# Kernel optimization log

Hardware: AMD Instinct MI355X
Metric: run time of the kernel (lower is better)

## Reference

```python
import jax, jax.numpy as jnp
import numpy as np
from jax import lax

N, S, H, L, E, V = 10000, 20, 512, 2, 100000, 10000


def setup_inputs() -> dict:
    key = jax.random.key(0)
    ks = jax.random.split(key, 12)
    return {
        "emb": jax.random.normal(ks[0], (V, H), jnp.float32),
        "W_ir": jax.random.normal(ks[1], (L, H, H), jnp.float32) * (2.0 / H) ** 0.5,
        "b_ir": jnp.ones((L, H), jnp.float32),
        "W_iz": jax.random.normal(ks[2], (L, H, H), jnp.float32) * (2.0 / H) ** 0.5,
        "b_iz": jnp.ones((L, H), jnp.float32),
        "lin_w": jax.random.normal(ks[3], (1, H), jnp.float32) * (1.0 / H) ** 0.5,
        "lin_b": jnp.zeros((1,), jnp.float32),
        "skip_w": jax.random.uniform(ks[4], (H, H), jnp.float32),
        "skip_b": jax.random.uniform(ks[5], (H,), jnp.float32),
        "walk_idx": jax.random.randint(ks[6], (N, S), 0, V),
        "edge_label_index": jax.random.randint(ks[7], (2, E), 0, N),
    }


def reference(emb, W_ir, b_ir, W_iz, b_iz, lin_w, lin_b, skip_w, skip_b,
              walk_idx, edge_label_index):
    x = emb[walk_idx]                       # [N, S, H]
    hn = jnp.zeros((x.shape[0], emb.shape[1]), x.dtype)
    for l in range(W_ir.shape[0]):
        # gates depend only on x, precompute all steps: F.linear(x, W) = x @ W.T
        h_all = jnp.einsum('nsh,kh->snk', x, W_ir[l]) + b_ir[l]          # [S, N, H]
        z_all = jax.nn.sigmoid(jnp.einsum('nsh,kh->snk', x, W_iz[l]) + b_iz[l])

        def step(h, tz):
            ht, zt = tz
            return (1.0 - zt) * h + zt * ht, None

        hn, _ = lax.scan(step, hn, (h_all, z_all))
    # note: F.dropout result in original is dead (overwritten); omitted
    score = jax.nn.sigmoid(hn @ lin_w.T + lin_b)        # [N, 1]
    node_feat = score[edge_label_index]                  # [2, E, 1]
    pred = jnp.sum(node_feat[0] * node_feat[1], axis=-1)  # [E] ('dot' decode)
    out2 = hn @ skip_w.T + skip_b                        # [N, H]
    return pred, out2
```

## Files before the change

### kernel.cpp

```cpp
#include <hip/hip_runtime.h>

#define H  512
#define NN 10000
#define SS 20
#define VV 100000
#define EE 100000

typedef __bf16 bf16x8 __attribute__((ext_vector_type(8)));
typedef float  f32x4  __attribute__((ext_vector_type(4)));

__device__ __forceinline__ unsigned short f2bf(float f) {
  unsigned u = __builtin_bit_cast(unsigned, f);
  u += 0x7FFFu + ((u >> 16) & 1u);
  return (unsigned short)(u >> 16);
}
__device__ __forceinline__ float bflo(int x) {
  return __builtin_bit_cast(float, (unsigned)x << 16);
}
__device__ __forceinline__ float bfhi(int x) {
  return __builtin_bit_cast(float, (unsigned)x & 0xFFFF0000u);
}
__device__ __forceinline__ float sigm(float x) { return 1.f / (1.f + __expf(-x)); }

__device__ __forceinline__ unsigned cpk(float lo, float hi) {
  unsigned r;
  asm("v_cvt_pk_bf16_f32 %0, %1, %2" : "=v"(r) : "v"(lo), "v"(hi));
  return r;
}
__device__ __forceinline__ void cvt_store8(unsigned short* dst, float4 a, float4 b) {
  int4 v;
  v.x = (int)cpk(a.x, a.y); v.y = (int)cpk(a.z, a.w);
  v.z = (int)cpk(b.x, b.y); v.w = (int)cpk(b.z, b.w);
  *(int4*)dst = v;
}
__device__ __forceinline__ bf16x8 cvt8(float4 a, float4 b) {
  int4 v;
  v.x = (int)cpk(a.x, a.y); v.y = (int)cpk(a.z, a.w);
  v.z = (int)cpk(b.x, b.y); v.w = (int)cpk(b.z, b.w);
  return __builtin_bit_cast(bf16x8, v);
}

__device__ __forceinline__ void pub_barrier() {
  asm volatile("s_waitcnt lgkmcnt(0)\n\ts_barrier" ::: "memory");
}

__launch_bounds__(256, 2)
__global__ void gru_fused(const float* __restrict__ emb,
                          const float* __restrict__ W_ir,
                          const float* __restrict__ W_iz,
                          const float* __restrict__ b_ir,
                          const float* __restrict__ b_iz,
                          const int* __restrict__ walk,
                          unsigned short* __restrict__ hnb) {
  __shared__ unsigned short As[4][80 * 64];
  __shared__ unsigned short hout[2][4][32];

  const int tid = threadIdx.x;
  const int w = tid >> 6, lane = tid & 63;
  const int r = lane & 15, q = lane >> 4;

  const int hwid = blockIdx.y * 16 + blockIdx.x;
  const int cg = (hwid >> 3) & 15;
  const int sb = ((hwid & 7) << 2) + (hwid >> 7);
  const int c0 = cg * 32;

  const int ly = r & 1;
  const int cch = c0 + 8 * w + (r >> 1);
  bf16x8 barr[2][16];
  float bias2[2];
  #pragma unroll
  for (int t = 0; t < 2; ++t) {
    const float* wrow = (t ? W_iz : W_ir) + (long)ly * H * H + (long)cch * H;
    #pragma unroll
    for (int u = 0; u < 16; ++u) {
      const float* s = wrow + u * 32 + q * 8;
      barr[t][u] = cvt8(*(const float4*)s, *(const float4*)(s + 4));
    }
    bias2[t] = (t ? b_iz : b_ir)[ly * H + cch];
  }

  const int row0 = tid >> 3, g0 = tid & 7;
  const int row1 = row0 + 32, row2 = row0 + 64;
  const bool has2 = (tid < 128);
  #define LMAP(m) (20 * (((m) >> 2) & 3) + 4 * ((m) >> 4) + ((m) & 3))
  #define SWZ(m)  ((m) * 64 + ((g0 ^ ((m) & 7)) * 8))
  const int L0 = LMAP(row0), L1 = LMAP(row1), L2 = LMAP(row2);
  const int sw0 = SWZ(row0), sw1 = SWZ(row1), sw2 = SWZ(row2);

  const int ngA = (2500 * sb) >> 5;
  const int ngB = (2500 * (sb + 1)) >> 5;

  int v0 = walk[ngA * 80 + L0]; v0 = ((unsigned)v0 < VV) ? v0 : 0;
  int v1 = walk[ngA * 80 + L1]; v1 = ((unsigned)v1 < VV) ? v1 : 0;
  int cur0 = v0 * H, cur1 = v1 * H, cur2 = 0;
  if (has2) { int v2 = walk[ngA * 80 + L2]; v2 = ((unsigned)v2 < VV) ? v2 : 0; cur2 = v2 * H; }

  float4 p0a[2], p0b[2], p1a[2], p1b[2], p2a[2], p2b[2];
  p2a[0] = p2a[1] = p2b[0] = p2b[1] = (float4){0, 0, 0, 0};

  {
    const float* s0 = emb + cur0 + g0 * 8;
    const float* s1 = emb + cur1 + g0 * 8;
    const float* s2 = emb + cur2 + g0 * 8;
    float4 a0 = *(const float4*)s0, b0 = *(const float4*)(s0 + 4);
    float4 a1 = *(const float4*)s1, b1 = *(const float4*)(s1 + 4);
    float4 a2 = {0,0,0,0}, b2 = {0,0,0,0};
    if (has2) { a2 = *(const float4*)s2; b2 = *(const float4*)(s2 + 4); }
    cvt_store8(&As[0][sw0], a0, b0);
    cvt_store8(&As[0][sw1], a1, b1);
    if (has2) cvt_store8(&As[0][sw2], a2, b2);
    a0 = *(const float4*)(s0 + 64); b0 = *(const float4*)(s0 + 68);
    a1 = *(const float4*)(s1 + 64); b1 = *(const float4*)(s1 + 68);
    if (has2) { a2 = *(const float4*)(s2 + 64); b2 = *(const float4*)(s2 + 68); }
    cvt_store8(&As[1][sw0], a0, b0);
    cvt_store8(&As[1][sw1], a1, b1);
    if (has2) cvt_store8(&As[1][sw2], a2, b2);
    p0a[0] = *(const float4*)(s0 + 128); p0b[0] = *(const float4*)(s0 + 132);
    p1a[0] = *(const float4*)(s1 + 128); p1b[0] = *(const float4*)(s1 + 132);
    if (has2) { p2a[0] = *(const float4*)(s2 + 128); p2b[0] = *(const float4*)(s2 + 132); }
  }

  f32x4 acc[5][2];
  const f32x4 fz = {0.f, 0.f, 0.f, 0.f};

  for (int ng = ngA; ng < ngB; ++ng) {
    #pragma unroll
    for (int mt = 0; mt < 5; ++mt)
      #pragma unroll
      for (int t = 0; t < 2; ++t) acc[mt][t] = fz;

    const int ngn = (ng + 1 < ngB) ? ng + 1 : ng;
    int n0 = walk[ngn * 80 + L0]; n0 = ((unsigned)n0 < VV) ? n0 : 0;
    int n1 = walk[ngn * 80 + L1]; n1 = ((unsigned)n1 < VV) ? n1 : 0;
    const int nxt0 = n0 * H, nxt1 = n1 * H;
    int nxt2 = 0;
    if (has2) { int n2 = walk[ngn * 80 + L2]; n2 = ((unsigned)n2 < VV) ? n2 : 0; nxt2 = n2 * H; }

    #pragma unroll
    for (int kc = 0; kc < 8; ++kc) {
      if ((kc & 1) == 0) pub_barrier();

      {
        const int cix = kc + 3;
        const int off = (cix & 7) * 64;
        const int u0 = (cix < 8) ? cur0 : nxt0;
        const int u1 = (cix < 8) ? cur1 : nxt1;
        const float* s0 = emb + u0 + off + g0 * 8;
        p0a[cix & 1] = *(const float4*)s0; p0b[cix & 1] = *(const float4*)(s0 + 4);
        const float* s1 = emb + u1 + off + g0 * 8;
        p1a[cix & 1] = *(const float4*)s1; p1b[cix & 1] = *(const float4*)(s1 + 4);
        if (has2) {
          const int u2 = (cix < 8) ? cur2 : nxt2;
          const float* s2 = emb + u2 + off + g0 * 8;
          p2a[cix & 1] = *(const float4*)s2; p2b[cix & 1] = *(const float4*)(s2 + 4);
        }
      }

      {
        unsigned short* An = &As[(kc + 2) & 3][0];
        cvt_store8(&An[sw0], p0a[kc & 1], p0b[kc & 1]);
        cvt_store8(&An[sw1], p1a[kc & 1], p1b[kc & 1]);
        if (has2) cvt_store8(&An[sw2], p2a[kc & 1], p2b[kc & 1]);
      }

      const unsigned short* Ab = &As[kc & 3][0];
      #pragma unroll
      for (int ks = 0; ks < 2; ++ks) {
        bf16x8 a[5];
        #pragma unroll
        for (int mt = 0; mt < 5; ++mt) {
          const int ar = mt * 16 + r;
          a[mt] = *(const bf16x8*)&Ab[ar * 64 + (((ks * 4 + q) ^ (ar & 7)) * 8)];
        }
        #pragma unroll
        for (int mt = 0; mt < 5; ++mt)
          #pragma unroll
          for (int t = 0; t < 2; ++t)
            acc[mt][t] = __builtin_amdgcn_mfma_f32_16x16x32_bf16(
                a[mt], barr[t][kc * 2 + ks], acc[mt][t], 0, 0, 0);
      }
    }

    {
      float hn1 = 0.f, a2 = 1.f, b2 = 0.f;
      #pragma unroll
      for (int s = 0; s < 20; ++s) {
        const float yh = acc[s >> 2][0][s & 3] + bias2[0];
        const float yz = acc[s >> 2][1][s & 3] + bias2[1];
        const float z = sigm(yz);
        hn1 += z * (yh - hn1);
        a2 *= (1.f - z);
        b2 += z * (yh - b2);
      }
      const float u2 = __shfl_xor(hn1, 1);
      if (ly == 1) hout[ng & 1][q][8 * w + (r >> 1)] = f2bf(a2 * u2 + b2);
    }
    pub_barrier();
    if (tid < 16) {
      const int nd = tid >> 2, seg = tid & 3;
      int4 v = *(const int4*)&hout[ng & 1][nd][seg * 8];
      *(int4*)(hnb + (long)(ng * 4 + nd) * 1024 + c0 + seg * 8) = v;
    }
    cur0 = nxt0; cur1 = nxt1; cur2 = nxt2;
  }
}

__global__ void score_kernel(const unsigned short* __restrict__ hnb,
                             const float* __restrict__ lin_w,
                             const float* __restrict__ lin_b,
                             float* __restrict__ R) {
  int tid = threadIdx.x;
  int wv = tid >> 6, lane = tid & 63;
  int node = blockIdx.x * 4 + wv;
  int k = lane * 8;
  int4 hv = *(const int4*)(hnb + (long)node * 1024 + k);
  float4 w0 = *(const float4*)(lin_w + k);
  float4 w1 = *(const float4*)(lin_w + k + 4);
  float s = bflo(hv.x) * w0.x + bfhi(hv.x) * w0.y + bflo(hv.y) * w0.z + bfhi(hv.y) * w0.w
          + bflo(hv.z) * w1.x + bfhi(hv.z) * w1.y + bflo(hv.w) * w1.z + bfhi(hv.w) * w1.w;
  #pragma unroll
  for (int off = 32; off > 0; off >>= 1) s += __shfl_down(s, off);
  if (lane == 0) R[256 + (long)node * 512] = sigm(s + lin_b[0]);
}

__global__ void pred_kernel(const int* __restrict__ eli, const float* __restrict__ R,
                            float* __restrict__ out) {
  int e = blockIdx.x * 256 + threadIdx.x;
  if (e < EE) {
    int a = eli[e];       a = (unsigned)a < NN ? a : 0;
    int b = eli[EE + e];  b = (unsigned)b < NN ? b : 0;
    out[e] = R[256 + (long)a * 512] * R[256 + (long)b * 512];
  }
}

__launch_bounds__(256)
__global__ void out2_kernel(const unsigned short* __restrict__ hnb,
                            const float* __restrict__ skip_w,
                            const float* __restrict__ skip_b,
                            float* __restrict__ out2) {
  __shared__ unsigned short Asl[32][520];
  __shared__ unsigned short Bsl[512][40];
  const int tid = threadIdx.x;
  const int lane = tid & 63, wv = tid >> 6;
  const int r = lane & 15, q = lane >> 4;
  const int m0 = blockIdx.x * 32;

  {
    int arow = tid >> 4;
    int acol = (tid & 15) * 32;
    #pragma unroll
    for (int hh = 0; hh < 2; ++hh) {
      int grow = m0 + hh * 16 + arow;
      unsigned short* dst = &Asl[hh * 16 + arow][acol];
      if (grow < NN) {
        const unsigned short* hr = hnb + (long)grow * 1024 + acol;
        *(int4*)(dst)      = *(const int4*)(hr);
        *(int4*)(dst + 8)  = *(const int4*)(hr + 8);
        *(int4*)(dst + 16) = *(const int4*)(hr + 16);
        *(int4*)(dst + 24) = *(const int4*)(hr + 24);
      } else {
        int4 z = {0, 0, 0, 0};
        *(int4*)(dst) = z; *(int4*)(dst + 8) = z;
        *(int4*)(dst + 16) = z; *(int4*)(dst + 24) = z;
      }
    }
  }

  const f32x4 fzero = {0.f, 0.f, 0.f, 0.f};
  f32x4 acc[2][8];
  #pragma unroll
  for (int rg = 0; rg < 2; ++rg)
    #pragma unroll
    for (int i = 0; i < 8; ++i) acc[rg][i] = fzero;

  const int ksub = (tid & 3) * 8;
  const int jb = tid >> 2;

  for (int k0 = 0; k0 < H; k0 += 32) {
    __syncthreads();
    #pragma unroll
    for (int it = 0; it < 8; ++it) {
      int jj = it * 64 + jb;
      const float* src = skip_w + (long)jj * H + k0 + ksub;
      cvt_store8(&Bsl[jj][ksub], *(const float4*)src, *(const float4*)(src + 4));
    }
    __syncthreads();
    bf16x8 af0 = *(const bf16x8*)&Asl[r][k0 + q * 8];
    bf16x8 af1 = *(const bf16x8*)&Asl[16 + r][k0 + q * 8];
    #pragma unroll
    for (int i = 0; i < 8; ++i) {
      bf16x8 bf = *(const bf16x8*)&Bsl[(wv * 8 + i) * 16 + r][q * 8];
      acc[0][i] = __builtin_amdgcn_mfma_f32_16x16x32_bf16(af0, bf, acc[0][i], 0, 0, 0);
      acc[1][i] = __builtin_amdgcn_mfma_f32_16x16x32_bf16(af1, bf, acc[1][i], 0, 0, 0);
    }
  }
  #pragma unroll
  for (int rg = 0; rg < 2; ++rg)
    #pragma unroll
    for (int i = 0; i < 8; ++i) {
      int col = (wv * 8 + i) * 16 + r;
      float sbv = skip_b[col];
      #pragma unroll
      for (int g = 0; g < 4; ++g) {
        int grow = m0 + rg * 16 + q * 4 + g;
        if (grow < NN) out2[(long)grow * H + col] = acc[rg][i][g] + sbv;
      }
    }
}

extern "C" void kernel_launch(void* const* d_in, const int* in_sizes, int n_in,
                              void* d_out, int out_size, void* d_ws, size_t ws_size,
                              hipStream_t stream) {
  const float* emb    = (const float*)d_in[0];
  const float* W_ir   = (const float*)d_in[1];
  const float* b_ir   = (const float*)d_in[2];
  const float* W_iz   = (const float*)d_in[3];
  const float* b_iz   = (const float*)d_in[4];
  const float* lin_w  = (const float*)d_in[5];
  const float* lin_b  = (const float*)d_in[6];
  const float* skip_w = (const float*)d_in[7];
  const float* skip_b = (const float*)d_in[8];
  const int*   walk   = (const int*)d_in[9];
  const int*   eli    = (const int*)d_in[10];
  float* out = (float*)d_out;
  float* R   = out + EE;
  unsigned short* hnb = (unsigned short*)R;

  dim3 g1(16, 32);
  gru_fused<<<g1, 256, 0, stream>>>(emb, W_ir, W_iz, b_ir, b_iz, walk, hnb);
  score_kernel<<<2500, 256, 0, stream>>>(hnb, lin_w, lin_b, R);
  pred_kernel<<<391, 256, 0, stream>>>(eli, R, out);
  out2_kernel<<<313, 256, 0, stream>>>(hnb, skip_w, skip_b, R);
}
```

Measured before the change: 680.2 us.

## Switch GRU gate GEMM to FP8 MFMA with more blocks per CU

Result: slower. 703.6 us (+3.4%).

```diff
diff --git a/kernel.cpp b/kernel.cpp
--- a/kernel.cpp
+++ b/kernel.cpp
@@ -33,18 +33,20 @@
   v.z = (int)cpk(b.x, b.y); v.w = (int)cpk(b.z, b.w);
   *(int4*)dst = v;
 }
-__device__ __forceinline__ bf16x8 cvt8(float4 a, float4 b) {
-  int4 v;
-  v.x = (int)cpk(a.x, a.y); v.y = (int)cpk(a.z, a.w);
-  v.z = (int)cpk(b.x, b.y); v.w = (int)cpk(b.z, b.w);
-  return __builtin_bit_cast(bf16x8, v);
+
+__device__ __forceinline__ uint2 cvt8_fp8(float4 a, float4 b) {
+  int x = __builtin_amdgcn_cvt_pk_fp8_f32(a.x, a.y, 0, false);
+  x = __builtin_amdgcn_cvt_pk_fp8_f32(a.z, a.w, x, true);
+  int y = __builtin_amdgcn_cvt_pk_fp8_f32(b.x, b.y, 0, false);
+  y = __builtin_amdgcn_cvt_pk_fp8_f32(b.z, b.w, y, true);
+  uint2 r; r.x = (unsigned)x; r.y = (unsigned)y; return r;
 }
 
 __device__ __forceinline__ void pub_barrier() {
   asm volatile("s_waitcnt lgkmcnt(0)\n\ts_barrier" ::: "memory");
 }
 
-__launch_bounds__(256, 2)
+__launch_bounds__(256, 3)
 __global__ void gru_fused(const float* __restrict__ emb,
                           const float* __restrict__ W_ir,
                           const float* __restrict__ W_iz,
@@ -52,7 +54,7 @@
                           const float* __restrict__ b_iz,
                           const int* __restrict__ walk,
                           unsigned short* __restrict__ hnb) {
-  __shared__ unsigned short As[4][80 * 64];
+  __shared__ __align__(16) unsigned char As[4][80 * 64];
   __shared__ unsigned short hout[2][4][32];
 
   const int tid = threadIdx.x;
@@ -60,13 +62,14 @@
   const int r = lane & 15, q = lane >> 4;
 
   const int hwid = blockIdx.y * 16 + blockIdx.x;
-  const int cg = (hwid >> 3) & 15;
-  const int sb = ((hwid & 7) << 2) + (hwid >> 7);
+  const int j = hwid >> 3;
+  const int cg = j & 15;
+  const int sb = (hwid & 7) * 6 + (j >> 4);
   const int c0 = cg * 32;
 
   const int ly = r & 1;
   const int cch = c0 + 8 * w + (r >> 1);
-  bf16x8 barr[2][16];
+  long long barr[2][16];
   float bias2[2];
   #pragma unroll
   for (int t = 0; t < 2; ++t) {
@@ -74,7 +77,8 @@
     #pragma unroll
     for (int u = 0; u < 16; ++u) {
       const float* s = wrow + u * 32 + q * 8;
-      barr[t][u] = cvt8(*(const float4*)s, *(const float4*)(s + 4));
+      uint2 v = cvt8_fp8(*(const float4*)s, *(const float4*)(s + 4));
+      barr[t][u] = __builtin_bit_cast(long long, v);
     }
     bias2[t] = (t ? b_iz : b_ir)[ly * H + cch];
   }
@@ -87,16 +91,15 @@
   const int L0 = LMAP(row0), L1 = LMAP(row1), L2 = LMAP(row2);
   const int sw0 = SWZ(row0), sw1 = SWZ(row1), sw2 = SWZ(row2);
 
-  const int ngA = (2500 * sb) >> 5;
-  const int ngB = (2500 * (sb + 1)) >> 5;
+  const int ngA = (2500 * sb) / 48;
+  const int ngB = (2500 * (sb + 1)) / 48;
 
   int v0 = walk[ngA * 80 + L0]; v0 = ((unsigned)v0 < VV) ? v0 : 0;
   int v1 = walk[ngA * 80 + L1]; v1 = ((unsigned)v1 < VV) ? v1 : 0;
   int cur0 = v0 * H, cur1 = v1 * H, cur2 = 0;
   if (has2) { int v2 = walk[ngA * 80 + L2]; v2 = ((unsigned)v2 < VV) ? v2 : 0; cur2 = v2 * H; }
 
-  float4 p0a[2], p0b[2], p1a[2], p1b[2], p2a[2], p2b[2];
-  p2a[0] = p2a[1] = p2b[0] = p2b[1] = (float4){0, 0, 0, 0};
+  float4 pa0, pb0, pa1, pb1, pa2 = {0,0,0,0}, pb2 = {0,0,0,0};
 
   {
     const float* s0 = emb + cur0 + g0 * 8;
@@ -106,19 +109,14 @@
     float4 a1 = *(const float4*)s1, b1 = *(const float4*)(s1 + 4);
     float4 a2 = {0,0,0,0}, b2 = {0,0,0,0};
     if (has2) { a2 = *(const float4*)s2; b2 = *(const float4*)(s2 + 4); }
-    cvt_store8(&As[0][sw0], a0, b0);
-    cvt_store8(&As[0][sw1], a1, b1);
-    if (has2) cvt_store8(&As[0][sw2], a2, b2);
-    a0 = *(const float4*)(s0 + 64); b0 = *(const float4*)(s0 + 68);
-    a1 = *(const float4*)(s1 + 64); b1 = *(const float4*)(s1 + 68);
-    if (has2) { a2 = *(const float4*)(s2 + 64); b2 = *(const float4*)(s2 + 68); }
-    cvt_store8(&As[1][sw0], a0, b0);
-    cvt_store8(&As[1][sw1], a1, b1);
-    if (has2) cvt_store8(&As[1][sw2], a2, b2);
-    p0a[0] = *(const float4*)(s0 + 128); p0b[0] = *(const float4*)(s0 + 132);
-    p1a[0] = *(const float4*)(s1 + 128); p1b[0] = *(const float4*)(s1 + 132);
-    if (has2) { p2a[0] = *(const float4*)(s2 + 128); p2b[0] = *(const float4*)(s2 + 132); }
-  }
+    *(uint2*)(&As[0][0] + sw0) = cvt8_fp8(a0, b0);
+    *(uint2*)(&As[0][0] + sw1) = cvt8_fp8(a1, b1);
+    if (has2) *(uint2*)(&As[0][0] + sw2) = cvt8_fp8(a2, b2);
+    pa0 = *(const float4*)(s0 + 64); pb0 = *(const float4*)(s0 + 68);
+    pa1 = *(const float4*)(s1 + 64); pb1 = *(const float4*)(s1 + 68);
+    if (has2) { pa2 = *(const float4*)(s2 + 64); pb2 = *(const float4*)(s2 + 68); }
+  }
+  pub_barrier();
 
   f32x4 acc[5][2];
   const f32x4 fz = {0.f, 0.f, 0.f, 0.f};
@@ -138,47 +136,44 @@
 
     #pragma unroll
     for (int kc = 0; kc < 8; ++kc) {
-      if ((kc & 1) == 0) pub_barrier();
-
       {
-        const int cix = kc + 3;
+        unsigned char* An = &As[(kc + 1) & 3][0];
+        *(uint2*)(An + sw0) = cvt8_fp8(pa0, pb0);
+        *(uint2*)(An + sw1) = cvt8_fp8(pa1, pb1);
+        if (has2) *(uint2*)(An + sw2) = cvt8_fp8(pa2, pb2);
+      }
+      {
+        const int cix = kc + 2;
         const int off = (cix & 7) * 64;
         const int u0 = (cix < 8) ? cur0 : nxt0;
         const int u1 = (cix < 8) ? cur1 : nxt1;
         const float* s0 = emb + u0 + off + g0 * 8;
-        p0a[cix & 1] = *(const float4*)s0; p0b[cix & 1] = *(const float4*)(s0 + 4);
+        pa0 = *(const float4*)s0; pb0 = *(const float4*)(s0 + 4);
         const float* s1 = emb + u1 + off + g0 * 8;
-        p1a[cix & 1] = *(const float4*)s1; p1b[cix & 1] = *(const float4*)(s1 + 4);
+        pa1 = *(const float4*)s1; pb1 = *(const float4*)(s1 + 4);
         if (has2) {
           const int u2 = (cix < 8) ? cur2 : nxt2;
           const float* s2 = emb + u2 + off + g0 * 8;
-          p2a[cix & 1] = *(const float4*)s2; p2b[cix & 1] = *(const float4*)(s2 + 4);
+          pa2 = *(const float4*)s2; pb2 = *(const float4*)(s2 + 4);
         }
       }
-
-      {
-        unsigned short* An = &As[(kc + 2) & 3][0];
-        cvt_store8(&An[sw0], p0a[kc & 1], p0b[kc & 1]);
-        cvt_store8(&An[sw1], p1a[kc & 1], p1b[kc & 1]);
-        if (has2) cvt_store8(&An[sw2], p2a[kc & 1], p2b[kc & 1]);
-      }
-
-      const unsigned short* Ab = &As[kc & 3][0];
+      const unsigned char* Ab = &As[kc & 3][0];
       #pragma unroll
       for (int ks = 0; ks < 2; ++ks) {
-        bf16x8 a[5];
+        long long a[5];
         #pragma unroll
         for (int mt = 0; mt < 5; ++mt) {
           const int ar = mt * 16 + r;
-          a[mt] = *(const bf16x8*)&Ab[ar * 64 + (((ks * 4 + q) ^ (ar & 7)) * 8)];
+          a[mt] = *(const long long*)(Ab + ar * 64 + (((ks * 4 + q) ^ (ar & 7)) * 8));
         }
         #pragma unroll
         for (int mt = 0; mt < 5; ++mt)
           #pragma unroll
           for (int t = 0; t < 2; ++t)
-            acc[mt][t] = __builtin_amdgcn_mfma_f32_16x16x32_bf16(
+            acc[mt][t] = __builtin_amdgcn_mfma_f32_16x16x32_fp8_fp8(
                 a[mt], barr[t][kc * 2 + ks], acc[mt][t], 0, 0, 0);
       }
+      pub_barrier();
     }
 
     {
@@ -326,7 +321,7 @@
   float* R   = out + EE;
   unsigned short* hnb = (unsigned short*)R;
 
-  dim3 g1(16, 32);
+  dim3 g1(16, 48);
   gru_fused<<<g1, 256, 0, stream>>>(emb, W_ir, W_iz, b_ir, b_iz, walk, hnb);
   score_kernel<<<2500, 256, 0, stream>>>(hnb, lin_w, lin_b, R);
   pred_kernel<<<391, 256, 0, stream>>>(eli, R, out);
```
